# Optimization experiments

Measured on AMD Instinct MI355X. Metric: run time of the kernel, lower is better.

## Reference

```python
import jax, jax.numpy as jnp
import numpy as np

B, H, S, D, E = 8, 12, 1024, 64, 8
NEG = 1000000.0  # mask penalty used by the original module

def setup_inputs() -> dict:
    key = jax.random.key(0)
    kq, kk, kv, kr, ki, km = jax.random.split(key, 6)
    Q = jax.random.normal(kq, (B, H, S, D), dtype=jnp.float32)
    K = jax.random.normal(kk, (B, H, S, D), dtype=jnp.float32)
    V = jax.random.normal(kv, (B, H, S, D), dtype=jnp.float32)
    route_mat = jax.random.uniform(kr, (B, E), dtype=jnp.float32)  # routing weights; grouping only
    ids = jax.random.randint(ki, (B,), 0, E, dtype=jnp.int64)       # expert id per sample
    mask = jax.random.randint(km, (B, S), 0, 2, dtype=jnp.int32)    # 1 = valid key position
    return {"Q": Q, "K": K, "V": V, "route_mat": route_mat, "ids": ids, "mask": mask}

def reference(Q, K, V, route_mat, ids, mask):
    # The torch module gathers batch samples per expert (ragged lists), runs
    # QK^T -> scale -> mask -> softmax -> (dropout p=0) -> @V per group, then
    # returns the grouped outputs. Grouping whole samples by expert is a pure
    # permutation of the batch, so the math equals per-sample attention; we
    # return results in the original batch order [B, H, S, D].
    scale = 1.0 / np.sqrt(D).astype(np.float32)
    maskf = mask.astype(Q.dtype)
    dot = jnp.einsum('bhqd,bhkd->bhqk', Q, K) * scale          # [B,H,S,S]
    dot = dot - NEG * (1.0 - maskf[:, None, None, :])
    attn = jax.nn.softmax(dot, axis=-1)
    return jnp.einsum('bhqk,bhkd->bhqd', attn, V)              # [B,H,S,D]
```

## Files before the change

### kernel.cpp

```cpp
#include <hip/hip_runtime.h>
#include <hip/hip_bf16.h>
#include <cstdint>
#include <cstddef>

#define HH 12
#define BH 96
#define SS 1024
#define DD 64
#define KT 64
#define QB 64
#define NQT (SS / QB)

typedef __attribute__((ext_vector_type(2))) float f32x2;
typedef __attribute__((ext_vector_type(4))) float f32x4;
typedef __attribute__((ext_vector_type(8))) short bf16x8;
typedef __attribute__((ext_vector_type(4))) int   i32x4;

#define SCL  0.1803368801111204f
#define NEGL 1442695.0f
#define THR  8.0f

__device__ __forceinline__ unsigned int pk2(float lo, float hi) {
    __hip_bfloat162 h = __float22bfloat162_rn(float2{lo, hi});
    unsigned int u;
    __builtin_memcpy(&u, &h, sizeof(u));
    return u;
}

__global__ __launch_bounds__(256) void prep_idx_kernel(
        const int* __restrict__ mask,
        int* __restrict__ idxbuf,
        int* __restrict__ nvalid) {
    __shared__ int sc[256];
    const int b   = blockIdx.x;
    const int tid = threadIdx.x;
    i32x4 m = *(const i32x4*)(mask + b * SS + tid * 4);
    int keep[4];
    int c = 0;
#pragma unroll
    for (int j = 0; j < 4; ++j) { keep[j] = (m[j] != 0); c += keep[j]; }
    sc[tid] = c;
    __syncthreads();
    for (int off = 1; off < 256; off <<= 1) {
        int v = (tid >= off) ? sc[tid - off] : 0;
        __syncthreads();
        sc[tid] += v;
        __syncthreads();
    }
    const int total = sc[255];
    int pos = sc[tid] - c;
    int* dst = idxbuf + b * SS;
    if (total == 0) {
#pragma unroll
        for (int j = 0; j < 4; ++j) dst[tid * 4 + j] = tid * 4 + j;
        if (tid == 0) nvalid[b] = SS;
        return;
    }
#pragma unroll
    for (int j = 0; j < 4; ++j)
        if (keep[j]) dst[pos++] = tid * 4 + j;
    const int padded = (total + 63) & ~63;
    for (int s = total + tid; s < padded; s += 256) dst[s] = 0;
    if (tid == 0) nvalid[b] = total;
}

__global__ __launch_bounds__(256, 4) void attn_kernel(
        const float* __restrict__ Q,
        const float* __restrict__ Kb,
        const float* __restrict__ Vb,
        const int* __restrict__ idxbuf,
        const int* __restrict__ nvalid,
        float* __restrict__ Out) {
    __shared__ unsigned short Klds[KT * DD];
    __shared__ unsigned short Vlds[DD * KT];
    __shared__ int idxLds[SS];

    const int tid  = threadIdx.x;
    const int w    = tid >> 6;
    const int lane = tid & 63;
    const int g    = lane >> 4;
    const int l15  = lane & 15;
    const int swq  = (l15 & 7) << 3;

    const int bh = blockIdx.x;
    const int qt = blockIdx.y;
    const int b  = bh / HH;

    ((i32x4*)idxLds)[tid] = ((const i32x4*)(idxbuf + b * SS))[tid];
    const int nv  = nvalid[b];
    const int NTb = (nv + 63) >> 6;

    bf16x8 qa[2];
    {
        const float* qp = Q + ((size_t)(bh * SS + qt * QB + w * 16 + l15)) * DD + 8 * g;
#pragma unroll
        for (int c = 0; c < 2; ++c) {
            f32x4 lo = *(const f32x4*)(qp + c * 32);
            f32x4 hi = *(const f32x4*)(qp + c * 32 + 4);
            union { bf16x8 v; unsigned int u[4]; } o;
            o.u[0] = pk2(lo[0] * SCL, lo[1] * SCL);
            o.u[1] = pk2(lo[2] * SCL, lo[3] * SCL);
            o.u[2] = pk2(hi[0] * SCL, hi[1] * SCL);
            o.u[3] = pk2(hi[2] * SCL, hi[3] * SCL);
            qa[c] = o.v;
        }
    }

    f32x4 kreg[2][2];
    f32x2 vreg[8];
    const int vd0 = (tid & 31) * 2;
    const int vk0 = (tid >> 5) * 8;
    auto load_tile_regs = [&](int t) {
#pragma unroll
        for (int i = 0; i < 2; ++i) {
            int c = tid + i * 256;
            int row = c >> 3, d0 = (c & 7) * 8;
            int krow = idxLds[t * KT + row];
            const float* kp = Kb + ((size_t)(bh * SS + krow)) * DD + d0;
            kreg[i][0] = *(const f32x4*)kp;
            kreg[i][1] = *(const f32x4*)(kp + 4);
        }
        {
            i32x4 vi0 = *(const i32x4*)&idxLds[t * KT + vk0];
            i32x4 vi1 = *(const i32x4*)&idxLds[t * KT + vk0 + 4];
            const float* vbase = Vb + (size_t)(bh * SS) * DD + vd0;
#pragma unroll
            for (int j = 0; j < 4; ++j) vreg[j]     = *(const f32x2*)(vbase + (size_t)vi0[j] * DD);
#pragma unroll
            for (int j = 0; j < 4; ++j) vreg[4 + j] = *(const f32x2*)(vbase + (size_t)vi1[j] * DD);
        }
    };
    auto write_tile_lds = [&]() {
#pragma unroll
        for (int i = 0; i < 2; ++i) {
            int c = tid + i * 256;
            int row = c >> 3, d0 = (c & 7) * 8;
            union { bf16x8 v; unsigned int u[4]; } kv;
            kv.u[0] = pk2(kreg[i][0][0], kreg[i][0][1]);
            kv.u[1] = pk2(kreg[i][0][2], kreg[i][0][3]);
            kv.u[2] = pk2(kreg[i][1][0], kreg[i][1][1]);
            kv.u[3] = pk2(kreg[i][1][2], kreg[i][1][3]);
            *(bf16x8*)&Klds[row * DD + (d0 ^ ((row & 7) << 3))] = kv.v;
        }
        {
            union { bf16x8 v; unsigned int u[4]; } v0, v1;
            v0.u[0] = pk2(vreg[0][0], vreg[1][0]);
            v0.u[1] = pk2(vreg[2][0], vreg[3][0]);
            v0.u[2] = pk2(vreg[4][0], vreg[5][0]);
            v0.u[3] = pk2(vreg[6][0], vreg[7][0]);
            v1.u[0] = pk2(vreg[0][1], vreg[1][1]);
            v1.u[1] = pk2(vreg[2][1], vreg[3][1]);
            v1.u[2] = pk2(vreg[4][1], vreg[5][1]);
            v1.u[3] = pk2(vreg[6][1], vreg[7][1]);
            *(bf16x8*)&Vlds[vd0 * KT + (vk0 ^ ((vd0 & 7) << 3))] = v0.v;
            *(bf16x8*)&Vlds[(vd0 + 1) * KT + (vk0 ^ (((vd0 + 1) & 7) << 3))] = v1.v;
        }
    };

    f32x4 Oacc0[4];
#pragma unroll
    for (int dt = 0; dt < 4; ++dt) Oacc0[dt] = (f32x4){0.f, 0.f, 0.f, 0.f};
    float m0 = -3.0e38f, l0 = 0.f;

    __syncthreads();
    load_tile_regs(0);

#define SOFTMAX_H(s, mr, lr, Oa, pk)                                          \
    do {                                                                      \
        float tmax;                                                           \
        {                                                                     \
            f32x4 mm = s[0];                                                  \
            _Pragma("unroll")                                                 \
            for (int n = 1; n < 4; ++n)                                       \
                _Pragma("unroll")                                             \
                for (int r = 0; r < 4; ++r) mm[r] = fmaxf(mm[r], s[n][r]);    \
            tmax = fmaxf(fmaxf(mm[0], mm[1]), fmaxf(mm[2], mm[3]));           \
        }                                                                     \
        tmax = fmaxf(tmax, __shfl_xor(tmax, 16));                             \
        tmax = fmaxf(tmax, __shfl_xor(tmax, 32));                             \
        if (!__all(tmax <= mr + THR)) {                                       \
            float mnew = fmaxf(mr, tmax);                                     \
            float corr = __builtin_amdgcn_exp2f(mr - mnew);                   \
            mr = mnew;                                                        \
            lr *= corr;                                                       \
            float cq[4];                                                      \
            _Pragma("unroll")                                                 \
            for (int r = 0; r < 4; ++r) cq[r] = __shfl(corr, 4 * g + r);      \
            _Pragma("unroll")                                                 \
            for (int dt = 0; dt < 4; ++dt)                                    \
                _Pragma("unroll")                                             \
                for (int r = 0; r < 4; ++r) Oa[dt][r] *= cq[r];               \
        }                                                                     \
        float tsum = 0.f;                                                     \
        _Pragma("unroll")                                                     \
        for (int n = 0; n < 4; ++n) {                                         \
            float p0 = __builtin_amdgcn_exp2f(s[n][0] - mr);                  \
            float p1 = __builtin_amdgcn_exp2f(s[n][1] - mr);                  \
            float p2 = __builtin_amdgcn_exp2f(s[n][2] - mr);                  \
            float p3 = __builtin_amdgcn_exp2f(s[n][3] - mr);                  \
            tsum += (p0 + p1) + (p2 + p3);                                    \
            pk[n][0] = pk2(p0, p1);                                           \
            pk[n][1] = pk2(p2, p3);                                           \
        }                                                                     \
        tsum += __shfl_xor(tsum, 16);                                         \
        tsum += __shfl_xor(tsum, 32);                                         \
        lr += tsum;                                                           \
    } while (0)

#define REBUILD_PA(pk, ks, pa)                                                \
    do {                                                                      \
        auto sw0 = __builtin_amdgcn_permlane32_swap(pk[2 * ks][0], pk[2 * ks + 1][0], false, false); \
        auto sw1 = __builtin_amdgcn_permlane32_swap(pk[2 * ks][1], pk[2 * ks + 1][1], false, false); \
        auto sp0 = __builtin_amdgcn_permlane16_swap(sw0[0], sw0[1], false, false); \
        auto sp1 = __builtin_amdgcn_permlane16_swap(sw1[0], sw1[1], false, false); \
        pa.u[0] = sp0[0];                                                     \
        pa.u[2] = sp0[1];                                                     \
        pa.u[1] = sp1[0];                                                     \
        pa.u[3] = sp1[1];                                                     \
    } while (0)

#define QKT_ONE(MMSTMT)                                                       \
    __builtin_amdgcn_s_setprio(1);                                            \
    _Pragma("unroll")                                                         \
    for (int n = 0; n < 4; ++n) {                                             \
        f32x4 mm; MMSTMT;                                                     \
        bf16x8 kb0 = *(const bf16x8*)&Klds[(16 * n + l15) * DD + ((8 * g) ^ swq)]; \
        bf16x8 kb1 = *(const bf16x8*)&Klds[(16 * n + l15) * DD + ((32 + 8 * g) ^ swq)]; \
        f32x4 a0 = __builtin_amdgcn_mfma_f32_16x16x32_bf16(kb0, qa[0], mm, 0, 0, 0); \
        s40[n]   = __builtin_amdgcn_mfma_f32_16x16x32_bf16(kb1, qa[1], a0, 0, 0, 0); \
    }                                                                         \
    __builtin_amdgcn_s_setprio(0);

#define SM_PV_ONE()                                                           \
    {                                                                         \
        unsigned int pk0[4][2];                                               \
        SOFTMAX_H(s40, m0, l0, Oacc0, pk0);                                   \
        __builtin_amdgcn_s_setprio(1);                                        \
        _Pragma("unroll")                                                     \
        for (int ks = 0; ks < 2; ++ks) {                                      \
            union { bf16x8 v; unsigned int u[4]; } pa0;                       \
            REBUILD_PA(pk0, ks, pa0);                                         \
            _Pragma("unroll")                                                 \
            for (int dt = 0; dt < 4; ++dt) {                                  \
                bf16x8 vb = *(const bf16x8*)                                  \
                    &Vlds[(dt * 16 + l15) * KT + ((ks * 32 + 8 * g) ^ swq)];  \
                Oacc0[dt] = __builtin_amdgcn_mfma_f32_16x16x32_bf16(pa0.v, vb, Oacc0[dt], 0, 0, 0); \
            }                                                                 \
        }                                                                     \
        __builtin_amdgcn_s_setprio(0);                                        \
    }

    for (int t = 0; t < NTb - 1; ++t) {
        __syncthreads();
        write_tile_lds();
        __syncthreads();
        load_tile_regs(t + 1);

        f32x4 s40[4];
        QKT_ONE({ mm[0] = 0.0f; mm[1] = 0.0f; mm[2] = 0.0f; mm[3] = 0.0f; });
        SM_PV_ONE();
    }

    {
        __syncthreads();
        write_tile_lds();
        __syncthreads();

        const int lastbase = (NTb - 1) * KT + 4 * g;
        f32x4 s40[4];
        QKT_ONE({
            int slot = lastbase + 16 * n;
            mm[0] = (slot + 0 < nv) ? 0.0f : -NEGL;
            mm[1] = (slot + 1 < nv) ? 0.0f : -NEGL;
            mm[2] = (slot + 2 < nv) ? 0.0f : -NEGL;
            mm[3] = (slot + 3 < nv) ? 0.0f : -NEGL;
        });
        SM_PV_ONE();
    }

    {
        float inv = 1.0f / l0;
        float invq[4];
#pragma unroll
        for (int r = 0; r < 4; ++r) invq[r] = __shfl(inv, 4 * g + r);
        const size_t rowbase = (size_t)(bh * SS + qt * QB + w * 16);
#pragma unroll
        for (int dt = 0; dt < 4; ++dt)
#pragma unroll
            for (int r = 0; r < 4; ++r)
                Out[(rowbase + 4 * g + r) * DD + dt * 16 + l15] = Oacc0[dt][r] * invq[r];
    }
}

extern "C" void kernel_launch(void* const* d_in, const int* in_sizes, int n_in,
                              void* d_out, int out_size, void* d_ws, size_t ws_size,
                              hipStream_t stream) {
    const float* Q   = (const float*)d_in[0];
    const float* K   = (const float*)d_in[1];
    const float* V   = (const float*)d_in[2];
    const int* mask  = (const int*)d_in[5];
    float* out       = (float*)d_out;

    int* idxbuf = (int*)d_ws;
    int* nvalid = idxbuf + 8 * SS;

    prep_idx_kernel<<<dim3(8), 256, 0, stream>>>(mask, idxbuf, nvalid);
    attn_kernel<<<dim3(BH, NQT), 256, 0, stream>>>(Q, K, V, idxbuf, nvalid, out);
}
```

Before: 47.89 us.

## Double query tile to 128 rows with 512-thread blocks sharing K/V tiles

Grows the query block from 64 to 128 rows and launches 512 threads (8 waves) per block, so each gathered K/V tile in LDS is reused by twice as many query rows. The K/V staging loads are redistributed so each thread loads one K chunk and one V column of 8 rows. This halves the block count and the redundant global K/V gathers, at the cost of fewer blocks (768) and more scalar V loads per thread. The launch bound hint asks for 6 blocks of 512 threads, which may constrain registers.

```diff
diff --git a/kernel.cpp b/kernel.cpp
--- a/kernel.cpp
+++ b/kernel.cpp
@@ -8,7 +8,7 @@
 #define SS 1024
 #define DD 64
 #define KT 64
-#define QB 64
+#define QB 128
 #define NQT (SS / QB)
 
 typedef __attribute__((ext_vector_type(2))) float f32x2;
@@ -64,7 +64,7 @@
     if (tid == 0) nvalid[b] = total;
 }
 
-__global__ __launch_bounds__(256, 4) void attn_kernel(
+__global__ __launch_bounds__(512, 6) void attn_kernel(
         const float* __restrict__ Q,
         const float* __restrict__ Kb,
         const float* __restrict__ Vb,
@@ -86,7 +86,8 @@
     const int qt = blockIdx.y;
     const int b  = bh / HH;
 
-    ((i32x4*)idxLds)[tid] = ((const i32x4*)(idxbuf + b * SS))[tid];
+    if (tid < 256)
+        ((i32x4*)idxLds)[tid] = ((const i32x4*)(idxbuf + b * SS))[tid];
     const int nv  = nvalid[b];
     const int NTb = (nv + 63) >> 6;
 
@@ -106,54 +107,44 @@
         }
     }
 
-    f32x4 kreg[2][2];
-    f32x2 vreg[8];
-    const int vd0 = (tid & 31) * 2;
-    const int vk0 = (tid >> 5) * 8;
+    f32x4 kreg[2];
+    float vreg[8];
+    const int krow_s = tid >> 3;
+    const int kd0    = (tid & 7) * 8;
+    const int vd     = lane;
+    const int vk0    = w * 8;
     auto load_tile_regs = [&](int t) {
-#pragma unroll
-        for (int i = 0; i < 2; ++i) {
-            int c = tid + i * 256;
-            int row = c >> 3, d0 = (c & 7) * 8;
-            int krow = idxLds[t * KT + row];
-            const float* kp = Kb + ((size_t)(bh * SS + krow)) * DD + d0;
-            kreg[i][0] = *(const f32x4*)kp;
-            kreg[i][1] = *(const f32x4*)(kp + 4);
-        }
         {
-            i32x4 vi0 = *(const i32x4*)&idxLds[t * KT + vk0];
-            i32x4 vi1 = *(const i32x4*)&idxLds[t * KT + vk0 + 4];
-            const float* vbase = Vb + (size_t)(bh * SS) * DD + vd0;
-#pragma unroll
-            for (int j = 0; j < 4; ++j) vreg[j]     = *(const f32x2*)(vbase + (size_t)vi0[j] * DD);
-#pragma unroll
-            for (int j = 0; j < 4; ++j) vreg[4 + j] = *(const f32x2*)(vbase + (size_t)vi1[j] * DD);
+            int krow = idxLds[t * KT + krow_s];
+            const float* kp = Kb + ((size_t)(bh * SS + krow)) * DD + kd0;
+            kreg[0] = *(const f32x4*)kp;
+            kreg[1] = *(const f32x4*)(kp + 4);
+        }
+        {
+            const float* vbase = Vb + (size_t)(bh * SS) * DD + vd;
+#pragma unroll
+            for (int j = 0; j < 8; ++j) {
+                int vrow = idxLds[t * KT + vk0 + j];
+                vreg[j] = vbase[(size_t)vrow * DD];
+            }
         }
     };
     auto write_tile_lds = [&]() {
-#pragma unroll
-        for (int i = 0; i < 2; ++i) {
-            int c = tid + i * 256;
-            int row = c >> 3, d0 = (c & 7) * 8;
+        {
             union { bf16x8 v; unsigned int u[4]; } kv;
-            kv.u[0] = pk2(kreg[i][0][0], kreg[i][0][1]);
-            kv.u[1] = pk2(kreg[i][0][2], kreg[i][0][3]);
-            kv.u[2] = pk2(kreg[i][1][0], kreg[i][1][1]);
-            kv.u[3] = pk2(kreg[i][1][2], kreg[i][1][3]);
-            *(bf16x8*)&Klds[row * DD + (d0 ^ ((row & 7) << 3))] = kv.v;
+            kv.u[0] = pk2(kreg[0][0], kreg[0][1]);
+            kv.u[1] = pk2(kreg[0][2], kreg[0][3]);
+            kv.u[2] = pk2(kreg[1][0], kreg[1][1]);
+            kv.u[3] = pk2(kreg[1][2], kreg[1][3]);
+            *(bf16x8*)&Klds[krow_s * DD + (kd0 ^ ((krow_s & 7) << 3))] = kv.v;
         }
         {
-            union { bf16x8 v; unsigned int u[4]; } v0, v1;
-            v0.u[0] = pk2(vreg[0][0], vreg[1][0]);
-            v0.u[1] = pk2(vreg[2][0], vreg[3][0]);
-            v0.u[2] = pk2(vreg[4][0], vreg[5][0]);
-            v0.u[3] = pk2(vreg[6][0], vreg[7][0]);
-            v1.u[0] = pk2(vreg[0][1], vreg[1][1]);
-            v1.u[1] = pk2(vreg[2][1], vreg[3][1]);
-            v1.u[2] = pk2(vreg[4][1], vreg[5][1]);
-            v1.u[3] = pk2(vreg[6][1], vreg[7][1]);
-            *(bf16x8*)&Vlds[vd0 * KT + (vk0 ^ ((vd0 & 7) << 3))] = v0.v;
-            *(bf16x8*)&Vlds[(vd0 + 1) * KT + (vk0 ^ (((vd0 + 1) & 7) << 3))] = v1.v;
+            union { bf16x8 v; unsigned int u[4]; } vv;
+            vv.u[0] = pk2(vreg[0], vreg[1]);
+            vv.u[1] = pk2(vreg[2], vreg[3]);
+            vv.u[2] = pk2(vreg[4], vreg[5]);
+            vv.u[3] = pk2(vreg[6], vreg[7]);
+            *(bf16x8*)&Vlds[vd * KT + (vk0 ^ ((vd & 7) << 3))] = vv.v;
         }
     };
 
@@ -305,5 +296,5 @@
     int* nvalid = idxbuf + 8 * SS;
 
     prep_idx_kernel<<<dim3(8), 256, 0, stream>>>(mask, idxbuf, nvalid);
-    attn_kernel<<<dim3(BH, NQT), 256, 0, stream>>>(Q, K, V, idxbuf, nvalid, out);
+    attn_kernel<<<dim3(BH, NQT), 512, 0, stream>>>(Q, K, V, idxbuf, nvalid, out);
 }
```

After: 42.83 us. 10.6% less time.
